# Kernel optimization log

Measured on AMD Instinct MI355X. Metric: run time of the kernel, lower is better.

The kernel has to match this reference:

```python
import jax, jax.numpy as jnp
import numpy as np

N_NODES = 10000
N_EDGES = 160000
IN_DIM = 512
HID_DIM = 512
OUT_DIM = 256
N_CLASSES = 8
N_GRAPHS = 64


def gcn_conv(x, W, b, src, dst, n):
    # PyG GCNConv: x @ W, add self-loops, symmetric normalization, scatter-add, + bias
    h = x @ W  # [N, out]
    loops = jnp.arange(n, dtype=src.dtype)
    src2 = jnp.concatenate([src, loops])
    dst2 = jnp.concatenate([dst, loops])
    deg = jax.ops.segment_sum(jnp.ones(src2.shape[0], h.dtype), dst2, num_segments=n)
    dinv = jnp.where(deg > 0, jax.lax.rsqrt(deg), 0.0)
    norm = dinv[src2] * dinv[dst2]          # [E+N]
    msgs = h[src2] * norm[:, None]          # gather + weight
    out = jax.ops.segment_sum(msgs, dst2, num_segments=n)  # scatter-add
    return out + b


def setup_inputs() -> dict:
    key = jax.random.key(0)
    ks = jax.random.split(key, 10)
    x = jax.random.normal(ks[0], (N_NODES, IN_DIM), dtype=jnp.float32)
    edge_index = jax.random.randint(ks[1], (2, N_EDGES), 0, N_NODES, dtype=jnp.int64)
    batch = jnp.sort(jax.random.randint(ks[2], (N_NODES,), 0, N_GRAPHS, dtype=jnp.int64))
    s = 0.02
    W1 = jax.random.normal(ks[3], (IN_DIM, HID_DIM), dtype=jnp.float32) * s
    b1 = jnp.zeros((HID_DIM,), jnp.float32)
    W2 = jax.random.normal(ks[4], (HID_DIM, OUT_DIM), dtype=jnp.float32) * s
    b2 = jnp.zeros((OUT_DIM,), jnp.float32)
    Wl = jax.random.normal(ks[5], (OUT_DIM, N_CLASSES), dtype=jnp.float32) * s
    bl = jnp.zeros((N_CLASSES,), jnp.float32)
    return {"x": x, "W1": W1, "b1": b1, "W2": W2, "b2": b2,
            "Wl": Wl, "bl": bl, "edge_index": edge_index, "batch": batch}


def reference(x, W1, b1, W2, b2, Wl, bl, edge_index, batch):
    src, dst = edge_index[0], edge_index[1]
    h = jax.nn.relu(gcn_conv(x, W1, b1, src, dst, N_NODES))
    # dropout(p=0.5) is identity at inference (training=False)
    h = jax.nn.relu(gcn_conv(h, W2, b2, src, dst, N_NODES))
    # global_mean_pool over graph ids
    sums = jax.ops.segment_sum(h, batch, num_segments=N_GRAPHS)
    cnts = jax.ops.segment_sum(jnp.ones((N_NODES,), h.dtype), batch, num_segments=N_GRAPHS)
    pooled = sums / jnp.maximum(cnts, 1.0)[:, None]  # [G, OUT_DIM]
    return pooled @ Wl + bl
```

## Files before the change

kernel.cpp:

```cpp
#include <hip/hip_runtime.h>

#define N_NODES   10000
#define IN_DIM    512
#define HID_DIM   512
#define OUT_DIM   256
#define N_CLASSES 8
#define N_GRAPHS  64

typedef __attribute__((ext_vector_type(8))) __bf16 bf16x8;
typedef __attribute__((ext_vector_type(4))) float f32x4;
typedef __attribute__((ext_vector_type(8))) unsigned short ushort8;
typedef __attribute__((ext_vector_type(4))) unsigned short ushort4v;

__device__ __forceinline__ unsigned short f2bf(float f) {
    union { float f; unsigned int u; } v; v.f = f;
    unsigned int r = v.u + 0x7FFFu + ((v.u >> 16) & 1u);
    return (unsigned short)(r >> 16);
}
__device__ __forceinline__ float bf2f(unsigned short u) {
    union { unsigned int u; float f; } v; v.u = ((unsigned int)u) << 16;
    return v.f;
}

__global__ void count_deg_kernel(const int* __restrict__ dst, int* __restrict__ cnt, int E) {
    int e = blockIdx.x * blockDim.x + threadIdx.x;
    if (e < E) atomicAdd(&cnt[dst[e]], 1);
}

__global__ void node_prep_kernel(const int* __restrict__ cnt, float* __restrict__ dinv, int n) {
    int i = blockIdx.x * blockDim.x + threadIdx.x;
    if (i < n) dinv[i] = rsqrtf((float)(cnt[i] + 1));
}

__global__ void bounds_kernel(const int* __restrict__ batch, int* __restrict__ start, int n) {
    int i = blockIdx.x * blockDim.x + threadIdx.x;
    if (i < n) {
        int b = batch[i];
        int bn = (i + 1 < n) ? batch[i + 1] : N_GRAPHS;
        for (int g = b + 1; g <= bn; g++) start[g] = i + 1;
        if (i == 0) for (int g = 0; g <= b; g++) start[g] = 0;
    }
}

__global__ __launch_bounds__(1024) void scan_kernel(const int* __restrict__ cnt,
                                                    int* __restrict__ offs,
                                                    int* __restrict__ pos, int n) {
    __shared__ int partial[1024];
    int tid = threadIdx.x;
    const int CH = (n + 1023) >> 10;
    int base = tid * CH;
    int s = 0;
    for (int i = 0; i < CH; i++) { int idx = base + i; if (idx < n) s += cnt[idx]; }
    partial[tid] = s;
    __syncthreads();
    for (int off = 1; off < 1024; off <<= 1) {
        int v = (tid >= off) ? partial[tid - off] : 0;
        __syncthreads();
        partial[tid] += v;
        __syncthreads();
    }
    int run = (tid > 0) ? partial[tid - 1] : 0;
    for (int i = 0; i < CH; i++) {
        int idx = base + i;
        if (idx < n) { offs[idx] = run; pos[idx] = run; run += cnt[idx]; }
    }
    if (tid == 0) offs[n] = partial[1023];
}

__global__ void fill_csr_kernel(const int* __restrict__ src, const int* __restrict__ dst,
                                const float* __restrict__ dinv, int* __restrict__ pos,
                                int* __restrict__ csrs, float* __restrict__ csrn, int E) {
    int e = blockIdx.x * blockDim.x + threadIdx.x;
    if (e < E) {
        int s = src[e], d = dst[e];
        int p = atomicAdd(&pos[d], 1);
        csrs[p] = s;
        csrn[p] = dinv[s] * dinv[d];
    }
}

__global__ __launch_bounds__(256) void transposeW_kernel(const float* __restrict__ W,
                                                         unsigned short* __restrict__ Wt,
                                                         int K, int N) {
    __shared__ float t[32][33];
    int bn = blockIdx.x * 32;
    int bk = blockIdx.y * 32;
    int tx = threadIdx.x, ty = threadIdx.y;
    #pragma unroll
    for (int j = 0; j < 32; j += 8)
        t[ty + j][tx] = W[(size_t)(bk + ty + j) * N + bn + tx];
    __syncthreads();
    #pragma unroll
    for (int j = 0; j < 32; j += 8)
        Wt[(size_t)(bn + ty + j) * K + bk + tx] = f2bf(t[tx][ty + j]);
}

template<int BM, int BN, bool A_F32, bool OUT_BF16>
__global__ __launch_bounds__(256) void mfma_gemm_kernel(const void* __restrict__ Ap,
                                                        const unsigned short* __restrict__ Bt,
                                                        void* __restrict__ Cp,
                                                        int M, int N, int K) {
    constexpr int BK = 32, PK = 40;
    constexpr int FM = BM / 32, FN = BN / 32;
    __shared__ unsigned short As[BM * PK];
    __shared__ unsigned short Bs[BN * PK];
    int tid  = threadIdx.x;
    int lane = tid & 63;
    int wid  = tid >> 6;
    int wm = wid >> 1, wn = wid & 1;
    int row0 = blockIdx.x * BM, col0 = blockIdx.y * BN;

    f32x4 acc[FM][FN] = {};

    for (int k0 = 0; k0 < K; k0 += BK) {
        #pragma unroll
        for (int i = 0; i < BM * 4 / 256; i++) {
            int l  = tid + i * 256;
            int r  = l >> 2;
            int cg = (l & 3) << 3;
            int gr = row0 + r;
            ushort8 av = {0, 0, 0, 0, 0, 0, 0, 0};
            if (A_F32) {
                const float* A = (const float*)Ap;
                if (gr < M) {
                    float4 f0 = *reinterpret_cast<const float4*>(&A[(size_t)gr * K + k0 + cg]);
                    float4 f1 = *reinterpret_cast<const float4*>(&A[(size_t)gr * K + k0 + cg + 4]);
                    av[0] = f2bf(f0.x); av[1] = f2bf(f0.y); av[2] = f2bf(f0.z); av[3] = f2bf(f0.w);
                    av[4] = f2bf(f1.x); av[5] = f2bf(f1.y); av[6] = f2bf(f1.z); av[7] = f2bf(f1.w);
                }
            } else {
                const unsigned short* A = (const unsigned short*)Ap;
                if (gr < M) av = *reinterpret_cast<const ushort8*>(&A[(size_t)gr * K + k0 + cg]);
            }
            *reinterpret_cast<ushort8*>(&As[r * PK + cg]) = av;
        }
        #pragma unroll
        for (int i = 0; i < BN * 4 / 256; i++) {
            int l  = tid + i * 256;
            int r  = l >> 2;
            int cg = (l & 3) << 3;
            *reinterpret_cast<ushort8*>(&Bs[r * PK + cg]) =
                *reinterpret_cast<const ushort8*>(&Bt[(size_t)(col0 + r) * K + k0 + cg]);
        }
        __syncthreads();
        int kk = (lane >> 4) << 3;
        int ra = (wm * (BM / 2) + (lane & 15)) * PK + kk;
        int rb = (wn * (BN / 2) + (lane & 15)) * PK + kk;
        bf16x8 a[FM], b[FN];
        #pragma unroll
        for (int m = 0; m < FM; m++)
            a[m] = *reinterpret_cast<const bf16x8*>(&As[ra + m * 16 * PK]);
        #pragma unroll
        for (int nn = 0; nn < FN; nn++)
            b[nn] = *reinterpret_cast<const bf16x8*>(&Bs[rb + nn * 16 * PK]);
        #pragma unroll
        for (int m = 0; m < FM; m++)
            #pragma unroll
            for (int nn = 0; nn < FN; nn++)
                acc[m][nn] = __builtin_amdgcn_mfma_f32_16x16x32_bf16(a[m], b[nn], acc[m][nn], 0, 0, 0);
        __syncthreads();
    }

    int rbase = row0 + wm * (BM / 2) + ((lane >> 4) << 2);
    int cbase = col0 + wn * (BN / 2) + (lane & 15);
    #pragma unroll
    for (int m = 0; m < FM; m++) {
        #pragma unroll
        for (int nn = 0; nn < FN; nn++) {
            #pragma unroll
            for (int j = 0; j < 4; j++) {
                int row = rbase + m * 16 + j;
                if (row < M) {
                    int col = cbase + nn * 16;
                    if (OUT_BF16) ((unsigned short*)Cp)[(size_t)row * N + col] = f2bf(acc[m][nn][j]);
                    else          ((float*)Cp)[(size_t)row * N + col] = acc[m][nn][j];
                }
            }
        }
    }
}

__global__ __launch_bounds__(256) void agg512_kernel(const unsigned short* __restrict__ h,
                                                     const int* __restrict__ offs,
                                                     const int* __restrict__ csrs,
                                                     const float* __restrict__ csrn,
                                                     const float* __restrict__ dinv,
                                                     const float* __restrict__ bias,
                                                     unsigned short* __restrict__ outp, int n) {
    int wid = threadIdx.x >> 6, lane = threadIdx.x & 63;
    int i = blockIdx.x * 4 + wid;
    if (i >= n) return;
    int f = lane * 8;
    float di = dinv[i], w0 = di * di;
    ushort8 hv = *reinterpret_cast<const ushort8*>(&h[(size_t)i * 512 + f]);
    float acc[8];
    #pragma unroll
    for (int j = 0; j < 8; j++) acc[j] = bf2f(hv[j]) * w0;
    int p0 = offs[i], p1 = offs[i + 1];
    if (p0 < p1) {
        int s = csrs[p0]; float w = csrn[p0];
        ushort8 v = *reinterpret_cast<const ushort8*>(&h[(size_t)s * 512 + f]);
        for (int p = p0 + 1; p < p1; p++) {
            int s2 = csrs[p]; float w2 = csrn[p];
            ushort8 v2 = *reinterpret_cast<const ushort8*>(&h[(size_t)s2 * 512 + f]);
            #pragma unroll
            for (int j = 0; j < 8; j++) acc[j] = fmaf(w, bf2f(v[j]), acc[j]);
            w = w2; v = v2;
        }
        #pragma unroll
        for (int j = 0; j < 8; j++) acc[j] = fmaf(w, bf2f(v[j]), acc[j]);
    }
    float4 b0 = *reinterpret_cast<const float4*>(&bias[f]);
    float4 b1 = *reinterpret_cast<const float4*>(&bias[f + 4]);
    ushort8 r;
    r[0] = f2bf(fmaxf(acc[0] + b0.x, 0.f)); r[1] = f2bf(fmaxf(acc[1] + b0.y, 0.f));
    r[2] = f2bf(fmaxf(acc[2] + b0.z, 0.f)); r[3] = f2bf(fmaxf(acc[3] + b0.w, 0.f));
    r[4] = f2bf(fmaxf(acc[4] + b1.x, 0.f)); r[5] = f2bf(fmaxf(acc[5] + b1.y, 0.f));
    r[6] = f2bf(fmaxf(acc[6] + b1.z, 0.f)); r[7] = f2bf(fmaxf(acc[7] + b1.w, 0.f));
    *reinterpret_cast<ushort8*>(&outp[(size_t)i * 512 + f]) = r;
}

__global__ __launch_bounds__(256) void agg256_kernel(const unsigned short* __restrict__ h,
                                                     const int* __restrict__ offs,
                                                     const int* __restrict__ csrs,
                                                     const float* __restrict__ csrn,
                                                     const float* __restrict__ dinv,
                                                     const float* __restrict__ bias,
                                                     unsigned short* __restrict__ outp, int n) {
    int wid = threadIdx.x >> 6, lane = threadIdx.x & 63;
    int i = blockIdx.x * 4 + wid;
    if (i >= n) return;
    int f = lane * 4;
    float di = dinv[i], w0 = di * di;
    ushort4v hv = *reinterpret_cast<const ushort4v*>(&h[(size_t)i * 256 + f]);
    float acc[4];
    #pragma unroll
    for (int j = 0; j < 4; j++) acc[j] = bf2f(hv[j]) * w0;
    int p0 = offs[i], p1 = offs[i + 1];
    if (p0 < p1) {
        int s = csrs[p0]; float w = csrn[p0];
        ushort4v v = *reinterpret_cast<const ushort4v*>(&h[(size_t)s * 256 + f]);
        for (int p = p0 + 1; p < p1; p++) {
            int s2 = csrs[p]; float w2 = csrn[p];
            ushort4v v2 = *reinterpret_cast<const ushort4v*>(&h[(size_t)s2 * 256 + f]);
            #pragma unroll
            for (int j = 0; j < 4; j++) acc[j] = fmaf(w, bf2f(v[j]), acc[j]);
            w = w2; v = v2;
        }
        #pragma unroll
        for (int j = 0; j < 4; j++) acc[j] = fmaf(w, bf2f(v[j]), acc[j]);
    }
    float4 bv = *reinterpret_cast<const float4*>(&bias[f]);
    ushort4v r;
    r[0] = f2bf(fmaxf(acc[0] + bv.x, 0.f)); r[1] = f2bf(fmaxf(acc[1] + bv.y, 0.f));
    r[2] = f2bf(fmaxf(acc[2] + bv.z, 0.f)); r[3] = f2bf(fmaxf(acc[3] + bv.w, 0.f));
    *reinterpret_cast<ushort4v*>(&outp[(size_t)i * 256 + f]) = r;
}

__global__ __launch_bounds__(256) void pool_head_kernel(const unsigned short* __restrict__ agg2b,
                                                        const int* __restrict__ start,
                                                        const float* __restrict__ Wl,
                                                        const float* __restrict__ bl,
                                                        float* __restrict__ out) {
    __shared__ float pooled[OUT_DIM];
    int g = blockIdx.x;
    int t = threadIdx.x;
    int s0 = start[g], s1 = start[g + 1];
    float sum = 0.f;
    for (int r = s0; r < s1; r++) sum += bf2f(agg2b[(size_t)r * OUT_DIM + t]);
    pooled[t] = sum / fmaxf((float)(s1 - s0), 1.0f);
    __syncthreads();
    int c = t >> 5, j = t & 31;
    float part = 0.f;
    #pragma unroll
    for (int m = 0; m < 8; m++) {
        int k = j + m * 32;
        part = fmaf(pooled[k], Wl[k * N_CLASSES + c], part);
    }
    #pragma unroll
    for (int m = 16; m >= 1; m >>= 1) part += __shfl_xor(part, m, 32);
    if (j == 0) out[g * N_CLASSES + c] = part + bl[c];
}

extern "C" void kernel_launch(void* const* d_in, const int* in_sizes, int n_in,
                              void* d_out, int out_size, void* d_ws, size_t ws_size,
                              hipStream_t stream) {
    const float* x   = (const float*)d_in[0];
    const float* W1  = (const float*)d_in[1];
    const float* b1  = (const float*)d_in[2];
    const float* W2  = (const float*)d_in[3];
    const float* b2  = (const float*)d_in[4];
    const float* Wl  = (const float*)d_in[5];
    const float* bl  = (const float*)d_in[6];
    const int*   ei  = (const int*)d_in[7];
    const int*   bat = (const int*)d_in[8];
    float* out = (float*)d_out;

    const int n = N_NODES;
    const int E = in_sizes[7] / 2;
    const int* src = ei;
    const int* dst = ei + E;

    unsigned short* h2b   = (unsigned short*)d_ws;
    unsigned short* agg2b = h2b + (size_t)n * OUT_DIM;
    unsigned short* h1b   = agg2b + (size_t)n * OUT_DIM;
    unsigned short* agg1b = h1b + (size_t)n * HID_DIM;
    unsigned short* W1t   = agg1b + (size_t)n * HID_DIM;
    unsigned short* W2t   = W1t + IN_DIM * HID_DIM;
    int*   cnt   = (int*)(W2t + HID_DIM * OUT_DIM);
    int*   offs  = cnt + n;
    int*   pos   = offs + n + 1;
    int*   csrs  = pos + n;
    float* csrn  = (float*)(csrs + E);
    float* dinv  = csrn + E;
    int*   start = (int*)(dinv + n);

    hipMemsetAsync(cnt, 0, n * sizeof(int), stream);

    count_deg_kernel<<<(E + 255) / 256, 256, 0, stream>>>(dst, cnt, E);
    node_prep_kernel<<<(n + 255) / 256, 256, 0, stream>>>(cnt, dinv, n);
    scan_kernel<<<1, 1024, 0, stream>>>(cnt, offs, pos, n);
    fill_csr_kernel<<<(E + 255) / 256, 256, 0, stream>>>(src, dst, dinv, pos, csrs, csrn, E);
    bounds_kernel<<<(n + 255) / 256, 256, 0, stream>>>(bat, start, n);

    transposeW_kernel<<<dim3(HID_DIM / 32, IN_DIM / 32), dim3(32, 8), 0, stream>>>(W1, W1t, IN_DIM, HID_DIM);
    transposeW_kernel<<<dim3(OUT_DIM / 32, HID_DIM / 32), dim3(32, 8), 0, stream>>>(W2, W2t, HID_DIM, OUT_DIM);

    dim3 g1((n + 127) / 128, HID_DIM / 64);
    mfma_gemm_kernel<128, 64, true, true><<<g1, 256, 0, stream>>>(x, W1t, h1b, n, HID_DIM, IN_DIM);
    agg512_kernel<<<(n + 3) / 4, 256, 0, stream>>>(h1b, offs, csrs, csrn, dinv, b1, agg1b, n);

    dim3 g2((n + 63) / 64, OUT_DIM / 64);
    mfma_gemm_kernel<64, 64, false, true><<<g2, 256, 0, stream>>>(agg1b, W2t, h2b, n, OUT_DIM, HID_DIM);
    agg256_kernel<<<(n + 3) / 4, 256, 0, stream>>>(h2b, offs, csrs, csrn, dinv, b2, agg2b, n);

    pool_head_kernel<<<N_GRAPHS, OUT_DIM, 0, stream>>>(agg2b, start, Wl, bl, out);
}
```

Measured before the change: 254.9 us.

## Merge prep kernels, pre-convert x to bf16, retile GEMM2, vectorize pooling

```diff
diff --git a/kernel.cpp b/kernel.cpp
--- a/kernel.cpp
+++ b/kernel.cpp
@@ -27,14 +27,11 @@
     if (e < E) atomicAdd(&cnt[dst[e]], 1);
 }
 
-__global__ void node_prep_kernel(const int* __restrict__ cnt, float* __restrict__ dinv, int n) {
-    int i = blockIdx.x * blockDim.x + threadIdx.x;
-    if (i < n) dinv[i] = rsqrtf((float)(cnt[i] + 1));
-}
-
-__global__ void bounds_kernel(const int* __restrict__ batch, int* __restrict__ start, int n) {
+__global__ void node_prep_kernel(const int* __restrict__ cnt, float* __restrict__ dinv,
+                                 const int* __restrict__ batch, int* __restrict__ start, int n) {
     int i = blockIdx.x * blockDim.x + threadIdx.x;
     if (i < n) {
+        dinv[i] = rsqrtf((float)(cnt[i] + 1));
         int b = batch[i];
         int bn = (i + 1 < n) ? batch[i + 1] : N_GRAPHS;
         for (int g = b + 1; g <= bn; g++) start[g] = i + 1;
@@ -79,13 +76,16 @@
     }
 }
 
-__global__ __launch_bounds__(256) void transposeW_kernel(const float* __restrict__ W,
-                                                         unsigned short* __restrict__ Wt,
-                                                         int K, int N) {
+__global__ __launch_bounds__(256) void transposeW2_kernel(const float* __restrict__ W1,
+                                                          unsigned short* __restrict__ W1t,
+                                                          const float* __restrict__ W2,
+                                                          unsigned short* __restrict__ W2t) {
     __shared__ float t[32][33];
-    int bn = blockIdx.x * 32;
-    int bk = blockIdx.y * 32;
-    int tx = threadIdx.x, ty = threadIdx.y;
+    int b = blockIdx.x;
+    const float* W; unsigned short* Wt; int K, N, bn, bk;
+    if (b < 256) { W = W1; Wt = W1t; K = IN_DIM;  N = HID_DIM; bn = (b & 15) * 32; bk = (b >> 4) * 32; }
+    else { b -= 256; W = W2; Wt = W2t; K = HID_DIM; N = OUT_DIM; bn = (b & 7) * 32;  bk = (b >> 3) * 32; }
+    int tx = threadIdx.x & 31, ty = threadIdx.x >> 5;
     #pragma unroll
     for (int j = 0; j < 32; j += 8)
         t[ty + j][tx] = W[(size_t)(bk + ty + j) * N + bn + tx];
@@ -95,8 +95,21 @@
         Wt[(size_t)(bn + ty + j) * K + bk + tx] = f2bf(t[tx][ty + j]);
 }
 
-template<int BM, int BN, bool A_F32, bool OUT_BF16>
-__global__ __launch_bounds__(256) void mfma_gemm_kernel(const void* __restrict__ Ap,
+__global__ __launch_bounds__(256) void cvt_x_kernel(const float* __restrict__ x,
+                                                    unsigned short* __restrict__ xb, int total8) {
+    int i = blockIdx.x * blockDim.x + threadIdx.x;
+    if (i < total8) {
+        float4 f0 = *reinterpret_cast<const float4*>(&x[(size_t)i * 8]);
+        float4 f1 = *reinterpret_cast<const float4*>(&x[(size_t)i * 8 + 4]);
+        ushort8 v;
+        v[0] = f2bf(f0.x); v[1] = f2bf(f0.y); v[2] = f2bf(f0.z); v[3] = f2bf(f0.w);
+        v[4] = f2bf(f1.x); v[5] = f2bf(f1.y); v[6] = f2bf(f1.z); v[7] = f2bf(f1.w);
+        *reinterpret_cast<ushort8*>(&xb[(size_t)i * 8]) = v;
+    }
+}
+
+template<int BM, int BN, bool OUT_BF16>
+__global__ __launch_bounds__(256) void mfma_gemm_kernel(const unsigned short* __restrict__ A,
                                                         const unsigned short* __restrict__ Bt,
                                                         void* __restrict__ Cp,
                                                         int M, int N, int K) {
@@ -120,18 +133,7 @@
             int cg = (l & 3) << 3;
             int gr = row0 + r;
             ushort8 av = {0, 0, 0, 0, 0, 0, 0, 0};
-            if (A_F32) {
-                const float* A = (const float*)Ap;
-                if (gr < M) {
-                    float4 f0 = *reinterpret_cast<const float4*>(&A[(size_t)gr * K + k0 + cg]);
-                    float4 f1 = *reinterpret_cast<const float4*>(&A[(size_t)gr * K + k0 + cg + 4]);
-                    av[0] = f2bf(f0.x); av[1] = f2bf(f0.y); av[2] = f2bf(f0.z); av[3] = f2bf(f0.w);
-                    av[4] = f2bf(f1.x); av[5] = f2bf(f1.y); av[6] = f2bf(f1.z); av[7] = f2bf(f1.w);
-                }
-            } else {
-                const unsigned short* A = (const unsigned short*)Ap;
-                if (gr < M) av = *reinterpret_cast<const ushort8*>(&A[(size_t)gr * K + k0 + cg]);
-            }
+            if (gr < M) av = *reinterpret_cast<const ushort8*>(&A[(size_t)gr * K + k0 + cg]);
             *reinterpret_cast<ushort8*>(&As[r * PK + cg]) = av;
         }
         #pragma unroll
@@ -262,20 +264,35 @@
                                                         const float* __restrict__ Wl,
                                                         const float* __restrict__ bl,
                                                         float* __restrict__ out) {
-    __shared__ float pooled[OUT_DIM];
+    __shared__ float smem[8][OUT_DIM];
     int g = blockIdx.x;
     int t = threadIdx.x;
+    int ry = t >> 5;
+    int cg = (t & 31) << 3;
     int s0 = start[g], s1 = start[g + 1];
-    float sum = 0.f;
-    for (int r = s0; r < s1; r++) sum += bf2f(agg2b[(size_t)r * OUT_DIM + t]);
-    pooled[t] = sum / fmaxf((float)(s1 - s0), 1.0f);
+    float acc[8] = {};
+    for (int r = s0 + ry; r < s1; r += 8) {
+        ushort8 v = *reinterpret_cast<const ushort8*>(&agg2b[(size_t)r * OUT_DIM + cg]);
+        #pragma unroll
+        for (int j = 0; j < 8; j++) acc[j] += bf2f(v[j]);
+    }
+    #pragma unroll
+    for (int j = 0; j < 8; j++) smem[ry][cg + j] = acc[j];
+    __syncthreads();
+    float inv = 1.0f / fmaxf((float)(s1 - s0), 1.0f);
+    float s = 0.f;
+    #pragma unroll
+    for (int r2 = 0; r2 < 8; r2++) s += smem[r2][t];
+    float pooled_t = s * inv;
+    __syncthreads();
+    smem[0][t] = pooled_t;
     __syncthreads();
     int c = t >> 5, j = t & 31;
     float part = 0.f;
     #pragma unroll
     for (int m = 0; m < 8; m++) {
         int k = j + m * 32;
-        part = fmaf(pooled[k], Wl[k * N_CLASSES + c], part);
+        part = fmaf(smem[0][k], Wl[k * N_CLASSES + c], part);
     }
     #pragma unroll
     for (int m = 16; m >= 1; m >>= 1) part += __shfl_xor(part, m, 32);
@@ -301,7 +318,8 @@
     const int* src = ei;
     const int* dst = ei + E;
 
-    unsigned short* h2b   = (unsigned short*)d_ws;
+    unsigned short* xb    = (unsigned short*)d_ws;
+    unsigned short* h2b   = xb + (size_t)n * IN_DIM;
     unsigned short* agg2b = h2b + (size_t)n * OUT_DIM;
     unsigned short* h1b   = agg2b + (size_t)n * OUT_DIM;
     unsigned short* agg1b = h1b + (size_t)n * HID_DIM;
@@ -318,20 +336,19 @@
     hipMemsetAsync(cnt, 0, n * sizeof(int), stream);
 
     count_deg_kernel<<<(E + 255) / 256, 256, 0, stream>>>(dst, cnt, E);
-    node_prep_kernel<<<(n + 255) / 256, 256, 0, stream>>>(cnt, dinv, n);
+    node_prep_kernel<<<(n + 255) / 256, 256, 0, stream>>>(cnt, dinv, bat, start, n);
     scan_kernel<<<1, 1024, 0, stream>>>(cnt, offs, pos, n);
     fill_csr_kernel<<<(E + 255) / 256, 256, 0, stream>>>(src, dst, dinv, pos, csrs, csrn, E);
-    bounds_kernel<<<(n + 255) / 256, 256, 0, stream>>>(bat, start, n);
-
-    transposeW_kernel<<<dim3(HID_DIM / 32, IN_DIM / 32), dim3(32, 8), 0, stream>>>(W1, W1t, IN_DIM, HID_DIM);
-    transposeW_kernel<<<dim3(OUT_DIM / 32, HID_DIM / 32), dim3(32, 8), 0, stream>>>(W2, W2t, HID_DIM, OUT_DIM);
+
+    transposeW2_kernel<<<384, 256, 0, stream>>>(W1, W1t, W2, W2t);
+    cvt_x_kernel<<<(n * IN_DIM / 8 + 255) / 256, 256, 0, stream>>>(x, xb, n * IN_DIM / 8);
 
     dim3 g1((n + 127) / 128, HID_DIM / 64);
-    mfma_gemm_kernel<128, 64, true, true><<<g1, 256, 0, stream>>>(x, W1t, h1b, n, HID_DIM, IN_DIM);
+    mfma_gemm_kernel<128, 64, true><<<g1, 256, 0, stream>>>(xb, W1t, h1b, n, HID_DIM, IN_DIM);
     agg512_kernel<<<(n + 3) / 4, 256, 0, stream>>>(h1b, offs, csrs, csrn, dinv, b1, agg1b, n);
 
-    dim3 g2((n + 63) / 64, OUT_DIM / 64);
-    mfma_gemm_kernel<64, 64, false, true><<<g2, 256, 0, stream>>>(agg1b, W2t, h2b, n, OUT_DIM, HID_DIM);
+    dim3 g2((n + 127) / 128, OUT_DIM / 64);
+    mfma_gemm_kernel<128, 64, true><<<g2, 256, 0, stream>>>(agg1b, W2t, h2b, n, OUT_DIM, HID_DIM);
     agg256_kernel<<<(n + 3) / 4, 256, 0, stream>>>(h2b, offs, csrs, csrn, dinv, b2, agg2b, n);
 
     pool_head_kernel<<<N_GRAPHS, OUT_DIM, 0, stream>>>(agg2b, start, Wl, bl, out);
```

Measured after the change: 213.7 us. 16.2% less time.
